# Kernel optimization log

Hardware: AMD Instinct MI355X
Metric: run time of the kernel (lower is better)

Reference implementation:

```python
import jax, jax.numpy as jnp
import numpy as np

B = 16      # number of point clouds
N = 4096    # points per cloud (max segment size, static)
D = 3       # xyz


def setup_inputs() -> dict:
    key = jax.random.key(0)
    k1, k2 = jax.random.split(key)
    pred = jax.random.normal(k1, (B * N, D), dtype=jnp.float32)
    target = jax.random.normal(k2, (B * N, D), dtype=jnp.float32)
    # sorted batch assignment with equal-size segments (so N_max is static)
    batch = jnp.repeat(jnp.arange(B, dtype=jnp.int64), N)
    return {"pred": pred, "target": target, "batch": batch}


def _to_dense_batch(x, batch):
    # Faithful to torch_geometric.utils.to_dense_batch: scatter each point into
    # its (cloud, within-cloud-position) slot; padding slots stay zero.
    T = x.shape[0]
    counts = jax.ops.segment_sum(jnp.ones((T,), jnp.int32), batch, num_segments=B)
    starts = jnp.concatenate([jnp.zeros((1,), jnp.int32), jnp.cumsum(counts)[:-1]])
    pos = jnp.arange(T, dtype=jnp.int32) - starts[batch]
    dense = jnp.zeros((B, N, x.shape[1]), x.dtype).at[batch, pos].set(x)
    return dense


def _chamfer(x, y):
    # pytorch3d.loss.chamfer_distance defaults: squared L2, point_reduction="mean",
    # batch_reduction="mean"; no lengths -> padded zeros count as points (as in source).
    x2 = jnp.sum(x * x, axis=-1)                      # [B, N]
    y2 = jnp.sum(y * y, axis=-1)                      # [B, N]
    xy = jnp.einsum("bid,bjd->bij", x, y)             # [B, N, N]
    d2 = x2[:, :, None] + y2[:, None, :] - 2.0 * xy   # [B, N, N] squared dists
    cham_x = jnp.mean(jnp.min(d2, axis=2), axis=1)    # x -> nearest y, mean over points
    cham_y = jnp.mean(jnp.min(d2, axis=1), axis=1)    # y -> nearest x
    return jnp.mean(cham_x + cham_y)                  # batch mean of summed directions


def reference(pred, target, batch):
    dense_x = _to_dense_batch(pred, batch)
    dense_y = _to_dense_batch(target, batch)
    return _chamfer(dense_x, dense_y)
```

## Files before the change

kernel.cpp:

```cpp
#include <hip/hip_runtime.h>


#define BB 16
#define NN 4096
#define T  256
#define M  8
#define S  8
#define YC (NN / S)
#define XT (NN / (T * M))

__global__ __launch_bounds__(T) void chamfer_partial(
    const float* __restrict__ pred,
    const float* __restrict__ target,
    unsigned int* __restrict__ pmin)
{
    __shared__ float4 ys[YC];

    const int b   = blockIdx.y;
    const int dir = blockIdx.z >> 3;
    const int yc  = blockIdx.z & 7;
    const float* xb = (dir ? target : pred) + (size_t)b * NN * 3;
    const float* yb = (dir ? pred : target) + (size_t)b * NN * 3 + (size_t)yc * YC * 3;

    for (int j = threadIdx.x; j < YC; j += T) {
        float y0 = yb[3 * j + 0];
        float y1 = yb[3 * j + 1];
        float y2 = yb[3 * j + 2];
        ys[j] = make_float4(-2.f * y0, -2.f * y1, -2.f * y2,
                            fmaf(y0, y0, fmaf(y1, y1, y2 * y2)));
    }
    __syncthreads();

    float x0[M], x1[M], x2[M], xsq[M], mn[M];
    const int xbase = blockIdx.x * (T * M);
#pragma unroll
    for (int m = 0; m < M; ++m) {
        int xi = xbase + threadIdx.x + m * T;
        float a = xb[3 * xi + 0];
        float c = xb[3 * xi + 1];
        float d = xb[3 * xi + 2];
        x0[m] = a; x1[m] = c; x2[m] = d;
        xsq[m] = fmaf(a, a, fmaf(c, c, d * d));
        mn[m]  = 3.402823466e38f;
    }

#pragma unroll 4
    for (int j = 0; j < YC; j += 2) {
        const float4 ya = ys[j];
        const float4 yv = ys[j + 1];
#pragma unroll
        for (int m = 0; m < M; ++m) {
            float fa = fmaf(x0[m], ya.x, fmaf(x1[m], ya.y, fmaf(x2[m], ya.z, ya.w)));
            float fb = fmaf(x0[m], yv.x, fmaf(x1[m], yv.y, fmaf(x2[m], yv.z, yv.w)));
            mn[m] = fminf(fminf(mn[m], fa), fb);
        }
    }

    const int obase = dir * (BB * NN) + b * NN + xbase + threadIdx.x;
#pragma unroll
    for (int m = 0; m < M; ++m) {
        float v = fmaxf(mn[m] + xsq[m], 0.f);
        atomicMin(&pmin[obase + m * T], __float_as_uint(v));
    }
}

#define TOTX (2 * BB * NN)

__global__ __launch_bounds__(256) void chamfer_reduce(
    const float* __restrict__ pmin, float* __restrict__ out)
{
    float s = 0.f;
    for (int i = blockIdx.x * 256 + threadIdx.x; i < TOTX; i += gridDim.x * 256)
        s += pmin[i];
#pragma unroll
    for (int off = 32; off > 0; off >>= 1)
        s += __shfl_down(s, off, 64);
    __shared__ float wsum[4];
    if ((threadIdx.x & 63) == 0) wsum[threadIdx.x >> 6] = s;
    __syncthreads();
    if (threadIdx.x == 0) {
        float t = wsum[0] + wsum[1] + wsum[2] + wsum[3];
        atomicAdd(out, t * (1.0f / (BB * NN)));
    }
}

extern "C" void kernel_launch(void* const* d_in, const int* in_sizes, int n_in,
                              void* d_out, int out_size, void* d_ws, size_t ws_size,
                              hipStream_t stream) {
    const float* pred   = (const float*)d_in[0];
    const float* target = (const float*)d_in[1];
    float* out = (float*)d_out;
    unsigned int* pmin = (unsigned int*)d_ws;

    hipMemsetAsync(pmin, 0x7f, (size_t)TOTX * sizeof(unsigned int), stream);
    hipMemsetAsync(out, 0, sizeof(float), stream);

    dim3 grid(XT, BB, 2 * S);
    chamfer_partial<<<grid, T, 0, stream>>>(pred, target, pmin);
    chamfer_reduce<<<128, 256, 0, stream>>>((const float*)pmin, out);
}
```

Before: 104.6 us.

## Compute pairwise distances with bf16 split-precision MFMA and fuse both directions

Replaces the scalar FMA distance loop with 32x32x16 bf16 MFMA tiles. Each coordinate and squared norm is split into hi/lo bf16 parts so the dot product keeps near-fp32 accuracy. The full distance matrix is computed once, and both the row minima (pred->target) and the column minima (target->pred, via LDS atomics) come from the same tile, which halves the pairwise work compared with computing each direction separately. The costs are extra min-reduction VALU work per MFMA output, cross-lane shuffles, atomics, and precision risk from the bf16 splitting.

```diff
diff --git a/kernel.cpp b/kernel.cpp
--- a/kernel.cpp
+++ b/kernel.cpp
@@ -1,67 +1,151 @@
 #include <hip/hip_runtime.h>
 
+
+typedef __attribute__((ext_vector_type(8))) short bf16x8;
+typedef __attribute__((ext_vector_type(16))) float floatx16;
 
 #define BB 16
 #define NN 4096
 #define T  256
-#define M  8
-#define S  8
-#define YC (NN / S)
-#define XT (NN / (T * M))
+#define NW 4
+#define RS 4
+#define XC (NW * RS * 32)
+#define YB 1024
+#define YT 32
+#define NT (YB / YT)
+#define ONEBF 0x3F80u
+#define FINF  0x7f7f7f7fu
 
-__global__ __launch_bounds__(T) void chamfer_partial(
+__device__ __forceinline__ unsigned int f2bf(float f) {
+    unsigned int u = __float_as_uint(f);
+    u += 0x7fffu + ((u >> 16) & 1u);
+    return u >> 16;
+}
+__device__ __forceinline__ float bf2f(unsigned int h) {
+    return __uint_as_float(h << 16);
+}
+
+__global__ __launch_bounds__(T, 2) void chamfer_mfma(
     const float* __restrict__ pred,
     const float* __restrict__ target,
     unsigned int* __restrict__ pmin)
 {
-    __shared__ float4 ys[YC];
+    __shared__ unsigned int lds_y[YB * 8];
+    __shared__ unsigned int lds_col[YB];
 
-    const int b   = blockIdx.y;
-    const int dir = blockIdx.z >> 3;
-    const int yc  = blockIdx.z & 7;
-    const float* xb = (dir ? target : pred) + (size_t)b * NN * 3;
-    const float* yb = (dir ? pred : target) + (size_t)b * NN * 3 + (size_t)yc * YC * 3;
+    const int b     = blockIdx.y;
+    const int xbase = blockIdx.x * XC;
+    const int ybase = blockIdx.z * YB;
+    const float* prd = pred   + (size_t)b * NN * 3;
+    const float* tgt = target + (size_t)b * NN * 3;
+    const int tid  = threadIdx.x;
+    const int lane = tid & 63, w = tid >> 6;
+    const int kg   = lane >> 5, m = lane & 31;
 
-    for (int j = threadIdx.x; j < YC; j += T) {
-        float y0 = yb[3 * j + 0];
-        float y1 = yb[3 * j + 1];
-        float y2 = yb[3 * j + 2];
-        ys[j] = make_float4(-2.f * y0, -2.f * y1, -2.f * y2,
-                            fmaf(y0, y0, fmaf(y1, y1, y2 * y2)));
+    for (int yl = tid; yl < YB; yl += T) {
+        const float* yp = tgt + (size_t)(ybase + yl) * 3;
+        float y0 = yp[0], y1 = yp[1], y2 = yp[2];
+        unsigned int h0 = f2bf(y0), h1 = f2bf(y1), h2 = f2bf(y2);
+        unsigned int H0 = f2bf(-2.f * bf2f(h0));
+        unsigned int H1 = f2bf(-2.f * bf2f(h1));
+        unsigned int H2 = f2bf(-2.f * bf2f(h2));
+        unsigned int L0 = f2bf(-2.f * (y0 - bf2f(h0)));
+        unsigned int L1 = f2bf(-2.f * (y1 - bf2f(h1)));
+        unsigned int L2 = f2bf(-2.f * (y2 - bf2f(h2)));
+        float ysq = fmaf(y0, y0, fmaf(y1, y1, y2 * y2));
+        unsigned int sh = f2bf(ysq);
+        unsigned int sl = f2bf(ysq - bf2f(sh));
+        unsigned int* r = &lds_y[yl * 8];
+        r[0] = H0 | (H1 << 16);
+        r[1] = H2 | (H0 << 16);
+        r[2] = H1 | (H2 << 16);
+        r[3] = L0 | (L1 << 16);
+        r[4] = L2 | (ONEBF << 16);
+        r[5] = ONEBF | (sh << 16);
+        r[6] = sl;
+        r[7] = 0;
+        lds_col[yl] = FINF;
+    }
+
+    unsigned int av[RS][4];
+#pragma unroll
+    for (int s = 0; s < RS; ++s) {
+        int xi = xbase + w * (RS * 32) + s * 32 + m;
+        const float* xp = prd + (size_t)xi * 3;
+        float x0 = xp[0], x1 = xp[1], x2 = xp[2];
+        unsigned int h0 = f2bf(x0), h1 = f2bf(x1), h2 = f2bf(x2);
+        unsigned int L0 = f2bf(x0 - bf2f(h0));
+        unsigned int L1 = f2bf(x1 - bf2f(h1));
+        unsigned int L2 = f2bf(x2 - bf2f(h2));
+        float xsq = fmaf(x0, x0, fmaf(x1, x1, x2 * x2));
+        unsigned int sh = f2bf(xsq);
+        unsigned int sl = f2bf(xsq - bf2f(sh));
+        av[s][0] = kg ? (h2 | (sh << 16))    : (h0 | (h1 << 16));
+        av[s][1] = kg ? (sl | (ONEBF << 16)) : (h2 | (L0 << 16));
+        av[s][2] = kg ? ONEBF                : (L1 | (L2 << 16));
+        av[s][3] = kg ? 0u                   : (h0 | (h1 << 16));
     }
     __syncthreads();
 
-    float x0[M], x1[M], x2[M], xsq[M], mn[M];
-    const int xbase = blockIdx.x * (T * M);
+    floatx16 acc[RS];
 #pragma unroll
-    for (int m = 0; m < M; ++m) {
-        int xi = xbase + threadIdx.x + m * T;
-        float a = xb[3 * xi + 0];
-        float c = xb[3 * xi + 1];
-        float d = xb[3 * xi + 2];
-        x0[m] = a; x1[m] = c; x2[m] = d;
-        xsq[m] = fmaf(a, a, fmaf(c, c, d * d));
-        mn[m]  = 3.402823466e38f;
+    for (int s = 0; s < RS; ++s)
+#pragma unroll
+        for (int r = 0; r < 16; ++r) acc[s][r] = 3.402823466e38f;
+    floatx16 zacc;
+#pragma unroll
+    for (int r = 0; r < 16; ++r) zacc[r] = 0.f;
+
+    union U { uint4 q; unsigned int u[4]; bf16x8 v; };
+    const uint4* yq = (const uint4*)lds_y;
+    uint4 bcur = yq[(0 * YT + m) * 2 + kg];
+    for (int t = 0; t < NT; ++t) {
+        int tn = (t + 1 < NT) ? t + 1 : t;
+        uint4 bnxt = yq[(tn * YT + m) * 2 + kg];
+        U bu; bu.q = bcur;
+        float cp = 3.402823466e38f;
+#pragma unroll
+        for (int s = 0; s < RS; ++s) {
+            U au;
+            au.u[0] = av[s][0]; au.u[1] = av[s][1];
+            au.u[2] = av[s][2]; au.u[3] = av[s][3];
+            floatx16 d = __builtin_amdgcn_mfma_f32_32x32x16_bf16(
+                au.v, bu.v, zacc, 0, 0, 0);
+            float e0 = fminf(d[0], d[1]),   e1 = fminf(d[2], d[3]);
+            float e2 = fminf(d[4], d[5]),   e3 = fminf(d[6], d[7]);
+            float e4 = fminf(d[8], d[9]),   e5 = fminf(d[10], d[11]);
+            float e6 = fminf(d[12], d[13]), e7 = fminf(d[14], d[15]);
+            float f0 = fminf(e0, e1), f1 = fminf(e2, e3);
+            float f2 = fminf(e4, e5), f3 = fminf(e6, e7);
+            cp = fminf(cp, fminf(fminf(f0, f1), fminf(f2, f3)));
+#pragma unroll
+            for (int r = 0; r < 16; ++r) acc[s][r] = fminf(acc[s][r], d[r]);
+        }
+        atomicMin(&lds_col[t * YT + m], __float_as_uint(fmaxf(cp, 0.f)));
+        bcur = bnxt;
     }
 
-#pragma unroll 4
-    for (int j = 0; j < YC; j += 2) {
-        const float4 ya = ys[j];
-        const float4 yv = ys[j + 1];
 #pragma unroll
-        for (int m = 0; m < M; ++m) {
-            float fa = fmaf(x0[m], ya.x, fmaf(x1[m], ya.y, fmaf(x2[m], ya.z, ya.w)));
-            float fb = fmaf(x0[m], yv.x, fmaf(x1[m], yv.y, fmaf(x2[m], yv.z, yv.w)));
-            mn[m] = fminf(fminf(mn[m], fa), fb);
+    for (int s = 0; s < RS; ++s) {
+#pragma unroll
+        for (int r = 0; r < 16; ++r) {
+            float v = acc[s][r];
+            v = fminf(v, __shfl_xor(v, 1, 64));
+            v = fminf(v, __shfl_xor(v, 2, 64));
+            v = fminf(v, __shfl_xor(v, 4, 64));
+            v = fminf(v, __shfl_xor(v, 8, 64));
+            v = fminf(v, __shfl_xor(v, 16, 64));
+            if (m == 0) {
+                int row = (r & 3) + 8 * (r >> 2) + 4 * kg;
+                int xi  = xbase + w * (RS * 32) + s * 32 + row;
+                atomicMin(&pmin[b * NN + xi], __float_as_uint(fmaxf(v, 0.f)));
+            }
         }
     }
 
-    const int obase = dir * (BB * NN) + b * NN + xbase + threadIdx.x;
-#pragma unroll
-    for (int m = 0; m < M; ++m) {
-        float v = fmaxf(mn[m] + xsq[m], 0.f);
-        atomicMin(&pmin[obase + m * T], __float_as_uint(v));
-    }
+    __syncthreads();
+    for (int yl = tid; yl < YB; yl += T)
+        atomicMin(&pmin[BB * NN + b * NN + ybase + yl], lds_col[yl]);
 }
 
 #define TOTX (2 * BB * NN)
@@ -95,7 +179,7 @@
     hipMemsetAsync(pmin, 0x7f, (size_t)TOTX * sizeof(unsigned int), stream);
     hipMemsetAsync(out, 0, sizeof(float), stream);
 
-    dim3 grid(XT, BB, 2 * S);
-    chamfer_partial<<<grid, T, 0, stream>>>(pred, target, pmin);
+    dim3 grid(NN / XC, BB, NN / YB);
+    chamfer_mfma<<<grid, T, 0, stream>>>(pred, target, pmin);
     chamfer_reduce<<<128, 256, 0, stream>>>((const float*)pmin, out);
 }
```

Measured after the change: 107.6 us. +2.9%, slower.
